# Performance work log

Hardware: AMD Instinct MI355X
Metric: run time of the kernel (lower is better)

## Reference

```python
import jax, jax.numpy as jnp
import numpy as np

# Uniform-scope sizes: B molecules, A atoms/mol, G fragments/mol, W map width,
# H hidden, L attention layers, S = G+1 (fg prompt row prepended per molecule)
B, A, G, W, H, L = 1024, 64, 31, 8, 512, 2
S = G + 1
DK = 32  # attention head dim (hard-coded in the module)


def _layernorm(x, g, b, eps):
    mu = jnp.mean(x, axis=-1, keepdims=True)
    var = jnp.var(x, axis=-1, keepdims=True)
    return g * (x - mu) * jax.lax.rsqrt(var + eps) + b


def setup_inputs() -> dict:
    key = jax.random.key(0)
    ks = jax.random.split(key, 16)
    s = 0.02
    return {
        "f_atom": jax.random.normal(ks[0], (B * A, H), jnp.float32),
        "f_group": jax.random.normal(ks[1], (B * G, H), jnp.float32),
        "fg": jax.random.normal(ks[2], (1, 3 * H), jnp.float32),
        "alpha": 0.1 * jnp.ones((1,), jnp.float32),
        "lr_w": jax.random.normal(ks[3], (3 * H, H), jnp.float32) * s,
        "lr_b": jnp.zeros((H,), jnp.float32),
        "wq_w": jax.random.normal(ks[4], (L, H, DK), jnp.float32) * s,
        "wq_b": jnp.zeros((L, DK), jnp.float32),
        "wk_w": jax.random.normal(ks[5], (L, H, DK), jnp.float32) * s,
        "wk_b": jnp.zeros((L, DK), jnp.float32),
        "wv_w": jax.random.normal(ks[6], (L, H, DK), jnp.float32) * s,
        "wv_b": jnp.zeros((L, DK), jnp.float32),
        "dense_w": jax.random.normal(ks[7], (L, DK, H), jnp.float32) * s,
        "dense_b": jnp.zeros((L, H), jnp.float32),
        "ln_g": jnp.ones((L, H), jnp.float32),
        "ln_b": jnp.zeros((L, H), jnp.float32),
        "lin_w": jax.random.normal(ks[8], (H, H), jnp.float32) * s,
        "lin_b": jnp.zeros((H,), jnp.float32),
        "norm_g": jnp.ones((H,), jnp.float32),
        "norm_b": jnp.zeros((H,), jnp.float32),
        "mapping": jax.random.randint(ks[9], (B * G, W), 0, A + 1, jnp.int64),
    }


def reference(f_atom, f_group, fg, alpha, lr_w, lr_b, wq_w, wq_b, wk_w, wk_b,
              wv_w, wv_b, dense_w, dense_b, ln_g, ln_b, lin_w, lin_b,
              norm_g, norm_b, mapping):
    # --- ragged gather + reduce + pad (vectorized: uniform scopes) ---
    a = f_atom.reshape(B, A, H)
    # prepend zero padding row per molecule (mapping index 0 -> zeros)
    a_pad = jnp.concatenate([jnp.zeros((B, 1, H), a.dtype), a], axis=1)  # [B,A+1,H]
    m = mapping.reshape(B, G, W)
    gathered = a_pad[jnp.arange(B)[:, None, None], m]  # [B,G,W,H]
    g = f_group.reshape(B, G, H)
    cur_g = jnp.concatenate(
        [gathered.sum(axis=2), gathered.max(axis=2), g], axis=-1)  # [B,G,3H]
    brics = jnp.concatenate(
        [jnp.broadcast_to(fg[None], (B, 1, 3 * H)), cur_g], axis=1)  # [B,S,3H]

    f_frag = jax.nn.relu(brics @ lr_w + lr_b)  # [B,S,H]

    # mask built from init_hiddens = f_frag (same for every layer)
    pm = (f_frag != 0).astype(f_frag.dtype)
    mask = jnp.einsum('bsh,bth->bst', pm, pm)  # [B,S,S]
    neg = jnp.asarray(-1e9, f_frag.dtype)
    scale = 1.0 / np.sqrt(DK)

    hs = f_frag
    attn = None
    for l in range(L):
        q = hs @ wq_w[l] + wq_b[l]
        k = hs @ wk_w[l] + wk_b[l]
        v = hs @ wv_w[l] + wv_b[l]
        scores = jnp.einsum('bsd,btd->bst', q, k) * scale
        scores = jnp.where(mask == 0, neg, scores)
        attn = jax.nn.softmax(scores, axis=-1)
        x = jnp.einsum('bst,btd->bsd', attn, v)
        dh = x @ dense_w[l] + dense_b[l]  # dropout is identity in eval
        hs = _layernorm(dh + hs, ln_g[l], ln_b[l], 1e-6)

    f_out = _layernorm(hs @ lin_w + lin_b, norm_g, norm_b, 1e-5) * alpha[0]
    return f_out[:, 0, :], attn
```

## Files before the change

kernel.cpp:

```cpp
#include <hip/hip_runtime.h>

#define B_   1024
#define A_   64
#define G_   31
#define W_   8
#define H_   512
#define L_   2
#define S_   32
#define DK_  32
#define K3H_ 1536

typedef short short8 __attribute__((ext_vector_type(8)));
typedef float floatx4 __attribute__((ext_vector_type(4)));

__device__ __forceinline__ float bf2f(unsigned short u){
  union { unsigned int i; float f; } x; x.i = ((unsigned int)u) << 16; return x.f;
}
__device__ __forceinline__ unsigned short f2bf(float f){
  union { float f; unsigned int i; } x; x.f = f;
  unsigned int u = x.i;
  return (unsigned short)((u + 0x7FFFu + ((u >> 16) & 1u)) >> 16);
}
__device__ __forceinline__ unsigned int pack2bf(float a, float b){
  return (unsigned int)f2bf(a) | ((unsigned int)f2bf(b) << 16);
}
__device__ __forceinline__ void gl_lds16(const unsigned short* g, unsigned short* l){
  __builtin_amdgcn_global_load_lds((const __attribute__((address_space(1))) unsigned int*)g,
                                   (__attribute__((address_space(3))) unsigned int*)l, 16, 0, 0);
}

__global__ __launch_bounds__(256) void prep_weights(
    const float* __restrict__ lr_w, const float* __restrict__ lin_w,
    const float* __restrict__ wq_w, const float* __restrict__ wk_w, const float* __restrict__ wv_w,
    const float* __restrict__ dense_w,
    unsigned short* __restrict__ lr_wT, unsigned short* __restrict__ lin_wT,
    unsigned short* __restrict__ qkvT, unsigned short* __restrict__ denseT){
  int bx = blockIdx.x;
  int tid = threadIdx.x;
  if (bx < 256){
    __shared__ float tile[64][65];
    const float* src; unsigned short* dst; int R, C;
    if (bx < 192){ src = lr_w;  dst = lr_wT;  R = 1536; C = 512; }
    else         { bx -= 192; src = lin_w; dst = lin_wT; R = 512;  C = 512; }
    int rt = bx >> 3, ct = bx & 7;
    int r16 = tid >> 4, c4 = tid & 15;
    #pragma unroll
    for (int p = 0; p < 4; ++p){
      int row = p*16 + r16;
      float4 v = *(const float4*)(src + (size_t)(rt*64 + row) * C + ct*64 + c4*4);
      tile[row][c4*4+0] = v.x; tile[row][c4*4+1] = v.y;
      tile[row][c4*4+2] = v.z; tile[row][c4*4+3] = v.w;
    }
    __syncthreads();
    int rr = tid >> 3, cc8 = tid & 7;
    #pragma unroll
    for (int p = 0; p < 2; ++p){
      int n = p*32 + rr;
      unsigned short o[8] __attribute__((aligned(16)));
      #pragma unroll
      for (int j = 0; j < 8; ++j) o[j] = f2bf(tile[cc8*8 + j][n]);
      *(uint4*)(dst + (size_t)(ct*64 + n) * R + rt*64 + cc8*8) = *(const uint4*)o;
    }
    return;
  }
  int i = (bx - 256) * 256 + tid;
  if (i < 98304){
    int k = i & 511; int t = i >> 9; int n = t & 31; int u = t >> 5;
    int p = u % 3, l = u / 3;
    const float* src = (p == 0) ? wq_w : (p == 1) ? wk_w : wv_w;
    qkvT[((size_t)((l*3+p)*S_ + n)) * H_ + k] = f2bf(src[((size_t)(l*H_ + k)) * DK_ + n]);
    return;
  }
  i -= 98304;
  if (i < 32768){
    int k = i & 31; int t = i >> 5; int n = t & 511; int l = t >> 9;
    denseT[((size_t)(l*H_ + n)) * DK_ + k] = f2bf(dense_w[((size_t)(l*DK_ + k)) * H_ + n]);
  }
}

__global__ __launch_bounds__(256) void build_brics(
    const float* __restrict__ f_atom, const float* __restrict__ f_group,
    const float* __restrict__ fg, const int* __restrict__ mapping,
    unsigned short* __restrict__ brics){
  __shared__ float atoms[64*128];
  int bx = blockIdx.x;
  int b = bx >> 2, qc = bx & 3;
  int kb = qc * 128;
  int tid = threadIdx.x;
  int wave = tid >> 6, lane = tid & 63;
  const float* fa = f_atom + (size_t)b * A_ * H_ + kb;

  #pragma unroll
  for (int j = 0; j < 8; ++j){
    int f = j*256 + tid;
    int r = f >> 5, c4v = f & 31;
    *(float4*)&atoms[r*128 + c4v*4] = *(const float4*)(fa + (size_t)r*H_ + c4v*4);
  }
  __syncthreads();

  int c2 = lane * 2;
  #pragma unroll
  for (int q = 0; q < 8; ++q){
    int s = wave*8 + q;
    unsigned short* out = brics + (size_t)(b*32 + s) * K3H_ + kb;
    if (s == 0){
      #pragma unroll
      for (int t3 = 0; t3 < 3; ++t3){
        const float* fgp = fg + t3*512 + kb + c2;
        *(unsigned int*)(out + t3*512 + c2) = pack2bf(fgp[0], fgp[1]);
      }
    } else {
      int g = s - 1;
      const int* mp = mapping + ((size_t)(b * G_ + g)) * W_;
      int4 m0 = *(const int4*)mp;
      int4 m1 = *(const int4*)(mp + 4);
      int id[8] = {m0.x, m0.y, m0.z, m0.w, m1.x, m1.y, m1.z, m1.w};
      float sum0 = 0.f, sum1 = 0.f;
      float mx0 = -3.4e38f, mx1 = -3.4e38f;
      #pragma unroll
      for (int w = 0; w < 8; ++w){
        int r = id[w] > 0 ? id[w] - 1 : 0;
        float2 v = *(const float2*)&atoms[r*128 + c2];
        bool z = (id[w] == 0);
        float v0 = z ? 0.f : v.x, v1 = z ? 0.f : v.y;
        sum0 += v0; sum1 += v1;
        mx0 = fmaxf(mx0, v0); mx1 = fmaxf(mx1, v1);
      }
      const float* gp = f_group + ((size_t)(b * G_ + g)) * H_ + kb + c2;
      float2 gv = *(const float2*)gp;
      *(unsigned int*)(out + c2)        = pack2bf(sum0, sum1);
      *(unsigned int*)(out + 512 + c2)  = pack2bf(mx0, mx1);
      *(unsigned int*)(out + 1024 + c2) = pack2bf(gv.x, gv.y);
    }
  }
}

__global__ __launch_bounds__(256) void gemm_frag(
    const unsigned short* __restrict__ brics, const unsigned short* __restrict__ wT,
    const float* __restrict__ lr_b, unsigned short* __restrict__ f_frag){
  __shared__ __align__(16) unsigned short As[128*64];
  __shared__ __align__(16) unsigned short Bs[128*64];
  int tid = threadIdx.x;
  int bx = blockIdx.x;
  int xcd = bx & 7, slot = bx >> 3;
  int mtile = xcd + 8 * (slot >> 2);
  int ntile = slot & 3;
  int rowStart = mtile * 128, colStart = ntile * 128;
  int lane = tid & 63, wave = tid >> 6;
  int m16 = lane & 15, quad = lane >> 4;
  int wm = wave >> 1, wn = wave & 1;
  floatx4 acc[4][4];
  #pragma unroll
  for (int i = 0; i < 4; ++i)
    #pragma unroll
    for (int j = 0; j < 4; ++j) acc[i][j] = (floatx4){0.f,0.f,0.f,0.f};

  int srow = tid >> 3;
  int gchunk = (tid & 7) ^ (srow & 7);
  size_t aOff[4], bOff[4];
  #pragma unroll
  for (int p = 0; p < 4; ++p){
    aOff[p] = (size_t)(rowStart + p*32 + srow) * K3H_ + gchunk*8;
    bOff[p] = (size_t)(colStart + p*32 + srow) * K3H_ + gchunk*8;
  }
  int fsw0 = ((0*4 + quad) ^ (m16 & 7)) * 8;
  int fsw1 = ((1*4 + quad) ^ (m16 & 7)) * 8;

  for (int kt = 0; kt < K3H_/64; ++kt){
    int kbase = kt * 64;
    #pragma unroll
    for (int p = 0; p < 4; ++p){
      gl_lds16(brics + aOff[p] + kbase, As + p*2048 + (size_t)tid*8);
      gl_lds16(wT    + bOff[p] + kbase, Bs + p*2048 + (size_t)tid*8);
    }
    __syncthreads();
    #pragma unroll
    for (int ks = 0; ks < 2; ++ks){
      int fsw = ks ? fsw1 : fsw0;
      short8 af[4], bfr[4];
      #pragma unroll
      for (int i = 0; i < 4; ++i){
        af[i]  = *(const short8*)(As + (wm*64 + i*16 + m16)*64 + fsw);
        bfr[i] = *(const short8*)(Bs + (wn*64 + i*16 + m16)*64 + fsw);
      }
      #pragma unroll
      for (int i = 0; i < 4; ++i)
        #pragma unroll
        for (int j = 0; j < 4; ++j)
          acc[i][j] = __builtin_amdgcn_mfma_f32_16x16x32_bf16(af[i], bfr[j], acc[i][j], 0, 0, 0);
    }
    __syncthreads();
  }
  #pragma unroll
  for (int i = 0; i < 4; ++i)
    #pragma unroll
    for (int j = 0; j < 4; ++j){
      int col = colStart + wn*64 + j*16 + m16;
      float bias = lr_b[col];
      #pragma unroll
      for (int r = 0; r < 4; ++r){
        int row = rowStart + wm*64 + i*16 + quad*4 + r;
        float v = acc[i][j][r] + bias;
        v = v > 0.f ? v : 0.f;
        f_frag[(size_t)row * H_ + col] = f2bf(v);
      }
    }
}

__global__ __launch_bounds__(256) void attn_kernel(
    const unsigned short* __restrict__ f_frag,
    const unsigned short* __restrict__ qkvT, const unsigned short* __restrict__ denseT,
    const float* __restrict__ wq_b, const float* __restrict__ wk_b, const float* __restrict__ wv_b,
    const float* __restrict__ dense_b, const float* __restrict__ ln_g, const float* __restrict__ ln_b,
    unsigned short* __restrict__ hsf, float* __restrict__ out_attn){
  const int HP = 544, TP = 40;
  __shared__ __align__(16) unsigned short hs[S_*544];
  __shared__ __align__(16) unsigned short Qs[S_*40];
  __shared__ __align__(16) unsigned short Ks[S_*40];
  __shared__ __align__(16) unsigned short Vt[S_*40];
  __shared__ __align__(16) unsigned short Ps[S_*40];
  __shared__ __align__(16) unsigned short Xs[S_*40];
  __shared__ unsigned long long pmask[S_*8];
  __shared__ unsigned int mz[S_];
  int b = blockIdx.x;
  int tid = threadIdx.x;
  int wave = tid >> 6, lane = tid & 63;
  int m16 = lane & 15, quad = lane >> 4;

  {
    int row = tid >> 3, cc = (tid & 7) * 64;
    const unsigned short* src = f_frag + ((size_t)(b * S_ + row)) * H_ + cc;
    unsigned short* dst = hs + row * HP + cc;
    #pragma unroll
    for (int k = 0; k < 64; k += 8)
      *(uint4*)(dst + k) = *(const uint4*)(src + k);
  }
  if (tid < S_) mz[tid] = 0u;
  __syncthreads();
  {
    int s = tid >> 3, w = tid & 7;
    unsigned long long m = 0ull;
    const unsigned short* hrow = hs + s * HP + w * 64;
    for (int j = 0; j < 64; ++j)
      if (hrow[j] != 0) m |= (1ull << j);
    pmask[s * 8 + w] = m;
  }
  __syncthreads();
  for (int idx = tid; idx < S_*S_; idx += 256){
    int s = idx >> 5, t2 = idx & 31;
    bool inter = false;
    #pragma unroll
    for (int w = 0; w < 8; ++w)
      inter = inter || ((pmask[s*8+w] & pmask[t2*8+w]) != 0ull);
    if (!inter) atomicOr(&mz[s], 1u << t2);
  }
  __syncthreads();

  const float scale = 0.17677669529663687f;
  for (int l = 0; l < L_; ++l){
    {
      int mt = wave >> 1, nt = wave & 1;
      floatx4 aq = {0,0,0,0}, ak = {0,0,0,0}, av = {0,0,0,0};
      const unsigned short* arow = hs + (mt*16 + m16) * HP + quad*8;
      const unsigned short* bq = qkvT + ((size_t)((l*3 + 0)*S_ + nt*16 + m16)) * H_ + quad*8;
      const unsigned short* bk = bq + (size_t)S_ * H_;
      const unsigned short* bv = bk + (size_t)S_ * H_;
      for (int k0 = 0; k0 < H_; k0 += 32){
        short8 a = *(const short8*)(arow + k0);
        aq = __builtin_amdgcn_mfma_f32_16x16x32_bf16(a, *(const short8*)(bq + k0), aq, 0,0,0);
        ak = __builtin_amdgcn_mfma_f32_16x16x32_bf16(a, *(const short8*)(bk + k0), ak, 0,0,0);
        av = __builtin_amdgcn_mfma_f32_16x16x32_bf16(a, *(const short8*)(bv + k0), av, 0,0,0);
      }
      int col = nt*16 + m16;
      float bqs = wq_b[l*DK_ + col], bks = wk_b[l*DK_ + col], bvs = wv_b[l*DK_ + col];
      #pragma unroll
      for (int r = 0; r < 4; ++r){
        int rw = mt*16 + quad*4 + r;
        Qs[rw*TP + col] = f2bf((aq[r] + bqs) * scale);
        Ks[rw*TP + col] = f2bf(ak[r] + bks);
        Vt[col*TP + rw] = f2bf(av[r] + bvs);
      }
    }
    __syncthreads();
    if (wave < 2){
      int mt = wave;
      short8 a  = *(const short8*)(Qs + (mt*16 + m16)*TP + quad*8);
      short8 b0 = *(const short8*)(Ks + m16*TP + quad*8);
      short8 b1 = *(const short8*)(Ks + (16 + m16)*TP + quad*8);
      floatx4 z = {0,0,0,0};
      floatx4 s0 = __builtin_amdgcn_mfma_f32_16x16x32_bf16(a, b0, z, 0,0,0);
      floatx4 s1 = __builtin_amdgcn_mfma_f32_16x16x32_bf16(a, b1, z, 0,0,0);
      #pragma unroll
      for (int r = 0; r < 4; ++r){
        int s = mt*16 + quad*4 + r;
        unsigned int m = mz[s];
        float v0 = ((m >> m16) & 1u) ? -1e9f : s0[r];
        float v1 = ((m >> (16 + m16)) & 1u) ? -1e9f : s1[r];
        float mx = fmaxf(v0, v1);
        #pragma unroll
        for (int d = 1; d < 16; d <<= 1) mx = fmaxf(mx, __shfl_xor(mx, d));
        float e0 = __expf(v0 - mx), e1 = __expf(v1 - mx);
        float sm = e0 + e1;
        #pragma unroll
        for (int d = 1; d < 16; d <<= 1) sm += __shfl_xor(sm, d);
        float inv = 1.f / sm;
        float p0 = e0 * inv, p1 = e1 * inv;
        Ps[s*TP + m16] = f2bf(p0);
        Ps[s*TP + 16 + m16] = f2bf(p1);
        if (l == L_ - 1){
          float* oa = out_attn + ((size_t)b * S_ + s) * S_;
          oa[m16] = p0; oa[16 + m16] = p1;
        }
      }
    }
    __syncthreads();
    {
      int mt = wave >> 1, nt = wave & 1;
      short8 a  = *(const short8*)(Ps + (mt*16 + m16)*TP + quad*8);
      short8 bv = *(const short8*)(Vt + (nt*16 + m16)*TP + quad*8);
      floatx4 z = {0,0,0,0};
      floatx4 x = __builtin_amdgcn_mfma_f32_16x16x32_bf16(a, bv, z, 0,0,0);
      #pragma unroll
      for (int r = 0; r < 4; ++r)
        Xs[(mt*16 + quad*4 + r)*TP + nt*16 + m16] = f2bf(x[r]);
    }
    __syncthreads();
    {
      short8 ax0 = *(const short8*)(Xs + m16*TP + quad*8);
      short8 ax1 = *(const short8*)(Xs + (16 + m16)*TP + quad*8);
      #pragma unroll
      for (int j = 0; j < 8; ++j){
        int col = (wave*8 + j)*16 + m16;
        short8 bw = *(const short8*)(denseT + ((size_t)(l*H_ + col)) * DK_ + quad*8);
        float db = dense_b[l*H_ + col];
        floatx4 z = {0,0,0,0};
        floatx4 d0 = __builtin_amdgcn_mfma_f32_16x16x32_bf16(ax0, bw, z, 0,0,0);
        floatx4 d1 = __builtin_amdgcn_mfma_f32_16x16x32_bf16(ax1, bw, z, 0,0,0);
        #pragma unroll
        for (int r = 0; r < 4; ++r){
          int row0 = quad*4 + r;
          float y0 = d0[r] + db + bf2f(hs[row0*HP + col]);
          hs[row0*HP + col] = f2bf(y0);
          int row1 = 16 + quad*4 + r;
          float y1 = d1[r] + db + bf2f(hs[row1*HP + col]);
          hs[row1*HP + col] = f2bf(y1);
        }
      }
    }
    __syncthreads();
    {
      #pragma unroll
      for (int rr = 0; rr < 8; ++rr){
        int row = wave*8 + rr;
        unsigned short* hrow = hs + row*HP + lane*8;
        short8 hv = *(const short8*)hrow;
        float v[8]; float s1 = 0.f, s2 = 0.f;
        #pragma unroll
        for (int j = 0; j < 8; ++j){ v[j] = bf2f((unsigned short)hv[j]); s1 += v[j]; s2 += v[j]*v[j]; }
        #pragma unroll
        for (int d = 1; d < 64; d <<= 1){ s1 += __shfl_xor(s1, d); s2 += __shfl_xor(s2, d); }
        float mean = s1 * (1.f/512.f);
        float var = s2 * (1.f/512.f) - mean*mean;
        float rs = rsqrtf(var + 1e-6f);
        unsigned short o[8] __attribute__((aligned(16)));
        #pragma unroll
        for (int j = 0; j < 8; ++j){
          int colj = lane*8 + j;
          float nv = (v[j] - mean) * rs * ln_g[l*H_ + colj] + ln_b[l*H_ + colj];
          o[j] = f2bf(nv);
        }
        *(uint4*)hrow = *(const uint4*)o;
      }
    }
    __syncthreads();
  }
  if (tid < 64){
    *(uint4*)(hsf + (size_t)b * H_ + tid*8) = *(const uint4*)(hs + tid*8);
  }
}

__global__ __launch_bounds__(256) void final_kernel(
    const unsigned short* __restrict__ hsf, const unsigned short* __restrict__ lin_wT,
    const float* __restrict__ lin_b, const float* __restrict__ norm_g, const float* __restrict__ norm_b,
    const float* __restrict__ alpha, float* __restrict__ out_f){
  const int HP = 544;
  __shared__ __align__(16) unsigned short hsb[32*544];
  int blk = blockIdx.x;
  int tid = threadIdx.x;
  int wave = tid >> 6, lane = tid & 63;
  int m16 = lane & 15, quad = lane >> 4;
  {
    int row = tid >> 3, cc = (tid & 7) * 64;
    const unsigned short* src = hsf + ((size_t)(blk*32 + row)) * H_ + cc;
    unsigned short* dst = hsb + row*HP + cc;
    #pragma unroll
    for (int k = 0; k < 64; k += 8)
      *(uint4*)(dst + k) = *(const uint4*)(src + k);
  }
  __syncthreads();
  floatx4 acc[2][8];
  #pragma unroll
  for (int mt = 0; mt < 2; ++mt)
    #pragma unroll
    for (int j = 0; j < 8; ++j) acc[mt][j] = (floatx4){0.f,0.f,0.f,0.f};
  for (int k0 = 0; k0 < H_; k0 += 32){
    short8 a0 = *(const short8*)(hsb + m16*HP + k0 + quad*8);
    short8 a1 = *(const short8*)(hsb + (16 + m16)*HP + k0 + quad*8);
    #pragma unroll
    for (int j = 0; j < 8; ++j){
      int n = (wave*8 + j)*16 + m16;
      short8 bw = *(const short8*)(lin_wT + (size_t)n * H_ + k0 + quad*8);
      acc[0][j] = __builtin_amdgcn_mfma_f32_16x16x32_bf16(a0, bw, acc[0][j], 0,0,0);
      acc[1][j] = __builtin_amdgcn_mfma_f32_16x16x32_bf16(a1, bw, acc[1][j], 0,0,0);
    }
  }
  __syncthreads();
  #pragma unroll
  for (int mt = 0; mt < 2; ++mt)
    #pragma unroll
    for (int j = 0; j < 8; ++j){
      int col = (wave*8 + j)*16 + m16;
      float lb = lin_b[col];
      #pragma unroll
      for (int r = 0; r < 4; ++r){
        int row = mt*16 + quad*4 + r;
        hsb[row*HP + col] = f2bf(acc[mt][j][r] + lb);
      }
    }
  __syncthreads();
  float al = alpha[0];
  #pragma unroll
  for (int rr = 0; rr < 8; ++rr){
    int row = wave*8 + rr;
    const unsigned short* hrow = hsb + row*HP + lane*8;
    short8 hv = *(const short8*)hrow;
    float v[8]; float s1 = 0.f, s2 = 0.f;
    #pragma unroll
    for (int j = 0; j < 8; ++j){ v[j] = bf2f((unsigned short)hv[j]); s1 += v[j]; s2 += v[j]*v[j]; }
    #pragma unroll
    for (int d = 1; d < 64; d <<= 1){ s1 += __shfl_xor(s1, d); s2 += __shfl_xor(s2, d); }
    float mean = s1 * (1.f/512.f);
    float var = s2 * (1.f/512.f) - mean*mean;
    float rs = rsqrtf(var + 1e-5f);
    float o[8];
    #pragma unroll
    for (int j = 0; j < 8; ++j){
      int colj = lane*8 + j;
      o[j] = ((v[j] - mean) * rs * norm_g[colj] + norm_b[colj]) * al;
    }
    float* op = out_f + ((size_t)(blk*32 + row)) * H_ + lane*8;
    float4 f0 = {o[0], o[1], o[2], o[3]};
    float4 f1 = {o[4], o[5], o[6], o[7]};
    *(float4*)op = f0;
    *(float4*)(op + 4) = f1;
  }
}

extern "C" void kernel_launch(void* const* d_in, const int* in_sizes, int n_in,
                              void* d_out, int out_size, void* d_ws, size_t ws_size,
                              hipStream_t stream){
  const float* f_atom  = (const float*)d_in[0];
  const float* f_group = (const float*)d_in[1];
  const float* fg      = (const float*)d_in[2];
  const float* alpha   = (const float*)d_in[3];
  const float* lr_w    = (const float*)d_in[4];
  const float* lr_b    = (const float*)d_in[5];
  const float* wq_w    = (const float*)d_in[6];
  const float* wq_b    = (const float*)d_in[7];
  const float* wk_w    = (const float*)d_in[8];
  const float* wk_b    = (const float*)d_in[9];
  const float* wv_w    = (const float*)d_in[10];
  const float* wv_b    = (const float*)d_in[11];
  const float* dense_w = (const float*)d_in[12];
  const float* dense_b = (const float*)d_in[13];
  const float* ln_g    = (const float*)d_in[14];
  const float* ln_b    = (const float*)d_in[15];
  const float* lin_w   = (const float*)d_in[16];
  const float* lin_b   = (const float*)d_in[17];
  const float* norm_g  = (const float*)d_in[18];
  const float* norm_b  = (const float*)d_in[19];
  const int*   mapping = (const int*)d_in[20];

  unsigned short* brics  = (unsigned short*)d_ws;
  unsigned short* f_frag = brics  + (size_t)32768 * 1536;
  unsigned short* lr_wT  = f_frag + (size_t)32768 * 512;
  unsigned short* qkvT   = lr_wT  + (size_t)512 * 1536;
  unsigned short* denseT = qkvT   + (size_t)2*3*32*512;
  unsigned short* lin_wT = denseT + (size_t)2*512*32;
  unsigned short* hsf    = lin_wT + (size_t)512*512;

  float* out_f    = (float*)d_out;
  float* out_attn = out_f + (size_t)B_ * H_;

  prep_weights<<<768, 256, 0, stream>>>(lr_w, lin_w, wq_w, wk_w, wv_w, dense_w,
                                        lr_wT, lin_wT, qkvT, denseT);
  build_brics<<<B_ * 4, 256, 0, stream>>>(f_atom, f_group, fg, mapping, brics);
  gemm_frag<<<(32768/128) * (512/128), 256, 0, stream>>>(brics, lr_wT, lr_b, f_frag);
  attn_kernel<<<B_, 256, 0, stream>>>(f_frag, qkvT, denseT, wq_b, wk_b, wv_b,
                                      dense_b, ln_g, ln_b, hsf, out_attn);
  final_kernel<<<B_/32, 256, 0, stream>>>(hsf, lin_wT, lin_b, norm_g, norm_b, alpha, out_f);
}
```

Measured before the change: 475.6 us.

## Merge weight prep with brics build and vectorize attention epilogue accesses

Folds the weight transposition/conversion kernel and the brics gather/reduce kernel into one launch with a shared LDS buffer, removing a kernel launch and letting the two independent workloads run concurrently. In the attention kernel, the nonzero-mask scan now uses 16-byte vector loads instead of scalar loads. The dense projection MFMA swaps its operands so each lane holds four consecutive columns, which allows 8-byte residual reads/writes and a float4 bias load instead of scattered scalar LDS accesses. The merged kernel's LDS footprint is set by the larger 32 KB brics buffer, which may limit occupancy for the transpose blocks.

```diff
diff --git a/kernel.cpp b/kernel.cpp
--- a/kernel.cpp
+++ b/kernel.cpp
@@ -29,27 +29,82 @@
                                    (__attribute__((address_space(3))) unsigned int*)l, 16, 0, 0);
 }
 
-__global__ __launch_bounds__(256) void prep_weights(
+__global__ __launch_bounds__(256) void prep_and_build(
+    const float* __restrict__ f_atom, const float* __restrict__ f_group,
+    const float* __restrict__ fg, const int* __restrict__ mapping,
     const float* __restrict__ lr_w, const float* __restrict__ lin_w,
     const float* __restrict__ wq_w, const float* __restrict__ wk_w, const float* __restrict__ wv_w,
     const float* __restrict__ dense_w,
+    unsigned short* __restrict__ brics,
     unsigned short* __restrict__ lr_wT, unsigned short* __restrict__ lin_wT,
     unsigned short* __restrict__ qkvT, unsigned short* __restrict__ denseT){
+  __shared__ __align__(16) float ldsf[8192];
   int bx = blockIdx.x;
   int tid = threadIdx.x;
-  if (bx < 256){
-    __shared__ float tile[64][65];
+
+  if (bx < 4096){
+    int b = bx >> 2, qc = bx & 3;
+    int kb = qc * 128;
+    int wave = tid >> 6, lane = tid & 63;
+    const float* fa = f_atom + (size_t)b * A_ * H_ + kb;
+    #pragma unroll
+    for (int j = 0; j < 8; ++j){
+      int f = j*256 + tid;
+      int r = f >> 5, c4v = f & 31;
+      *(float4*)&ldsf[r*128 + c4v*4] = *(const float4*)(fa + (size_t)r*H_ + c4v*4);
+    }
+    __syncthreads();
+    int c2 = lane * 2;
+    #pragma unroll
+    for (int q = 0; q < 8; ++q){
+      int s = wave*8 + q;
+      unsigned short* out = brics + (size_t)(b*32 + s) * K3H_ + kb;
+      if (s == 0){
+        #pragma unroll
+        for (int t3 = 0; t3 < 3; ++t3){
+          const float* fgp = fg + t3*512 + kb + c2;
+          *(unsigned int*)(out + t3*512 + c2) = pack2bf(fgp[0], fgp[1]);
+        }
+      } else {
+        int g = s - 1;
+        const int* mp = mapping + ((size_t)(b * G_ + g)) * W_;
+        int4 m0 = *(const int4*)mp;
+        int4 m1 = *(const int4*)(mp + 4);
+        int id[8] = {m0.x, m0.y, m0.z, m0.w, m1.x, m1.y, m1.z, m1.w};
+        float sum0 = 0.f, sum1 = 0.f;
+        float mx0 = -3.4e38f, mx1 = -3.4e38f;
+        #pragma unroll
+        for (int w = 0; w < 8; ++w){
+          int r = id[w] > 0 ? id[w] - 1 : 0;
+          float2 v = *(const float2*)&ldsf[r*128 + c2];
+          bool z = (id[w] == 0);
+          float v0 = z ? 0.f : v.x, v1 = z ? 0.f : v.y;
+          sum0 += v0; sum1 += v1;
+          mx0 = fmaxf(mx0, v0); mx1 = fmaxf(mx1, v1);
+        }
+        const float* gp = f_group + ((size_t)(b * G_ + g)) * H_ + kb + c2;
+        float2 gv = *(const float2*)gp;
+        *(unsigned int*)(out + c2)        = pack2bf(sum0, sum1);
+        *(unsigned int*)(out + 512 + c2)  = pack2bf(mx0, mx1);
+        *(unsigned int*)(out + 1024 + c2) = pack2bf(gv.x, gv.y);
+      }
+    }
+    return;
+  }
+
+  if (bx < 4352){
+    int tb = bx - 4096;
     const float* src; unsigned short* dst; int R, C;
-    if (bx < 192){ src = lr_w;  dst = lr_wT;  R = 1536; C = 512; }
-    else         { bx -= 192; src = lin_w; dst = lin_wT; R = 512;  C = 512; }
-    int rt = bx >> 3, ct = bx & 7;
+    if (tb < 192){ src = lr_w;  dst = lr_wT;  R = 1536; C = 512; }
+    else         { tb -= 192; src = lin_w; dst = lin_wT; R = 512;  C = 512; }
+    int rt = tb >> 3, ct = tb & 7;
     int r16 = tid >> 4, c4 = tid & 15;
     #pragma unroll
     for (int p = 0; p < 4; ++p){
       int row = p*16 + r16;
       float4 v = *(const float4*)(src + (size_t)(rt*64 + row) * C + ct*64 + c4*4);
-      tile[row][c4*4+0] = v.x; tile[row][c4*4+1] = v.y;
-      tile[row][c4*4+2] = v.z; tile[row][c4*4+3] = v.w;
+      ldsf[row*65 + c4*4+0] = v.x; ldsf[row*65 + c4*4+1] = v.y;
+      ldsf[row*65 + c4*4+2] = v.z; ldsf[row*65 + c4*4+3] = v.w;
     }
     __syncthreads();
     int rr = tid >> 3, cc8 = tid & 7;
@@ -58,12 +113,13 @@
       int n = p*32 + rr;
       unsigned short o[8] __attribute__((aligned(16)));
       #pragma unroll
-      for (int j = 0; j < 8; ++j) o[j] = f2bf(tile[cc8*8 + j][n]);
+      for (int j = 0; j < 8; ++j) o[j] = f2bf(ldsf[(cc8*8 + j)*65 + n]);
       *(uint4*)(dst + (size_t)(ct*64 + n) * R + rt*64 + cc8*8) = *(const uint4*)o;
     }
     return;
   }
-  int i = (bx - 256) * 256 + tid;
+
+  int i = (bx - 4352) * 256 + tid;
   if (i < 98304){
     int k = i & 511; int t = i >> 9; int n = t & 31; int u = t >> 5;
     int p = u % 3, l = u / 3;
@@ -75,63 +131,6 @@
   if (i < 32768){
     int k = i & 31; int t = i >> 5; int n = t & 511; int l = t >> 9;
     denseT[((size_t)(l*H_ + n)) * DK_ + k] = f2bf(dense_w[((size_t)(l*DK_ + k)) * H_ + n]);
-  }
-}
-
-__global__ __launch_bounds__(256) void build_brics(
-    const float* __restrict__ f_atom, const float* __restrict__ f_group,
-    const float* __restrict__ fg, const int* __restrict__ mapping,
-    unsigned short* __restrict__ brics){
-  __shared__ float atoms[64*128];
-  int bx = blockIdx.x;
-  int b = bx >> 2, qc = bx & 3;
-  int kb = qc * 128;
-  int tid = threadIdx.x;
-  int wave = tid >> 6, lane = tid & 63;
-  const float* fa = f_atom + (size_t)b * A_ * H_ + kb;
-
-  #pragma unroll
-  for (int j = 0; j < 8; ++j){
-    int f = j*256 + tid;
-    int r = f >> 5, c4v = f & 31;
-    *(float4*)&atoms[r*128 + c4v*4] = *(const float4*)(fa + (size_t)r*H_ + c4v*4);
-  }
-  __syncthreads();
-
-  int c2 = lane * 2;
-  #pragma unroll
-  for (int q = 0; q < 8; ++q){
-    int s = wave*8 + q;
-    unsigned short* out = brics + (size_t)(b*32 + s) * K3H_ + kb;
-    if (s == 0){
-      #pragma unroll
-      for (int t3 = 0; t3 < 3; ++t3){
-        const float* fgp = fg + t3*512 + kb + c2;
-        *(unsigned int*)(out + t3*512 + c2) = pack2bf(fgp[0], fgp[1]);
-      }
-    } else {
-      int g = s - 1;
-      const int* mp = mapping + ((size_t)(b * G_ + g)) * W_;
-      int4 m0 = *(const int4*)mp;
-      int4 m1 = *(const int4*)(mp + 4);
-      int id[8] = {m0.x, m0.y, m0.z, m0.w, m1.x, m1.y, m1.z, m1.w};
-      float sum0 = 0.f, sum1 = 0.f;
-      float mx0 = -3.4e38f, mx1 = -3.4e38f;
-      #pragma unroll
-      for (int w = 0; w < 8; ++w){
-        int r = id[w] > 0 ? id[w] - 1 : 0;
-        float2 v = *(const float2*)&atoms[r*128 + c2];
-        bool z = (id[w] == 0);
-        float v0 = z ? 0.f : v.x, v1 = z ? 0.f : v.y;
-        sum0 += v0; sum1 += v1;
-        mx0 = fmaxf(mx0, v0); mx1 = fmaxf(mx1, v1);
-      }
-      const float* gp = f_group + ((size_t)(b * G_ + g)) * H_ + kb + c2;
-      float2 gv = *(const float2*)gp;
-      *(unsigned int*)(out + c2)        = pack2bf(sum0, sum1);
-      *(unsigned int*)(out + 512 + c2)  = pack2bf(mx0, mx1);
-      *(unsigned int*)(out + 1024 + c2) = pack2bf(gv.x, gv.y);
-    }
   }
 }
 
@@ -239,10 +238,15 @@
   __syncthreads();
   {
     int s = tid >> 3, w = tid & 7;
+    const unsigned short* hrow = hs + s * HP + w * 64;
     unsigned long long m = 0ull;
-    const unsigned short* hrow = hs + s * HP + w * 64;
-    for (int j = 0; j < 64; ++j)
-      if (hrow[j] != 0) m |= (1ull << j);
+    #pragma unroll
+    for (int c = 0; c < 64; c += 8){
+      short8 hv = *(const short8*)(hrow + c);
+      #pragma unroll
+      for (int j = 0; j < 8; ++j)
+        if ((unsigned short)hv[j] != 0) m |= (1ull << (c + j));
+    }
     pmask[s * 8 + w] = m;
   }
   __syncthreads();
@@ -326,25 +330,32 @@
     }
     __syncthreads();
     {
-      short8 ax0 = *(const short8*)(Xs + m16*TP + quad*8);
-      short8 ax1 = *(const short8*)(Xs + (16 + m16)*TP + quad*8);
+      short8 bx0 = *(const short8*)(Xs + m16*TP + quad*8);
+      short8 bx1 = *(const short8*)(Xs + (16 + m16)*TP + quad*8);
       #pragma unroll
       for (int j = 0; j < 8; ++j){
-        int col = (wave*8 + j)*16 + m16;
-        short8 bw = *(const short8*)(denseT + ((size_t)(l*H_ + col)) * DK_ + quad*8);
-        float db = dense_b[l*H_ + col];
+        int dct = wave*8 + j;
+        short8 aw = *(const short8*)(denseT + ((size_t)(l*H_ + dct*16 + m16)) * DK_ + quad*8);
         floatx4 z = {0,0,0,0};
-        floatx4 d0 = __builtin_amdgcn_mfma_f32_16x16x32_bf16(ax0, bw, z, 0,0,0);
-        floatx4 d1 = __builtin_amdgcn_mfma_f32_16x16x32_bf16(ax1, bw, z, 0,0,0);
+        floatx4 d0 = __builtin_amdgcn_mfma_f32_16x16x32_bf16(aw, bx0, z, 0,0,0);
+        floatx4 d1 = __builtin_amdgcn_mfma_f32_16x16x32_bf16(aw, bx1, z, 0,0,0);
+        int dc0 = dct*16 + quad*4;
+        float4 db4 = *(const float4*)(dense_b + l*H_ + dc0);
+        const float dbr[4] = {db4.x, db4.y, db4.z, db4.w};
+        unsigned short* h0 = hs + m16*HP + dc0;
+        unsigned short* h1 = hs + (16 + m16)*HP + dc0;
+        unsigned long long u0 = *(unsigned long long*)h0;
+        unsigned long long u1 = *(unsigned long long*)h1;
+        unsigned long long o0 = 0ull, o1 = 0ull;
         #pragma unroll
         for (int r = 0; r < 4; ++r){
-          int row0 = quad*4 + r;
-          float y0 = d0[r] + db + bf2f(hs[row0*HP + col]);
-          hs[row0*HP + col] = f2bf(y0);
-          int row1 = 16 + quad*4 + r;
-          float y1 = d1[r] + db + bf2f(hs[row1*HP + col]);
-          hs[row1*HP + col] = f2bf(y1);
+          float hv0 = bf2f((unsigned short)(u0 >> (16*r)));
+          float hv1 = bf2f((unsigned short)(u1 >> (16*r)));
+          o0 |= (unsigned long long)f2bf(d0[r] + dbr[r] + hv0) << (16*r);
+          o1 |= (unsigned long long)f2bf(d1[r] + dbr[r] + hv1) << (16*r);
         }
+        *(unsigned long long*)h0 = o0;
+        *(unsigned long long*)h1 = o1;
       }
     }
     __syncthreads();
@@ -492,9 +503,9 @@
   float* out_f    = (float*)d_out;
   float* out_attn = out_f + (size_t)B_ * H_;
 
-  prep_weights<<<768, 256, 0, stream>>>(lr_w, lin_w, wq_w, wk_w, wv_w, dense_w,
-                                        lr_wT, lin_wT, qkvT, denseT);
-  build_brics<<<B_ * 4, 256, 0, stream>>>(f_atom, f_group, fg, mapping, brics);
+  prep_and_build<<<4864, 256, 0, stream>>>(f_atom, f_group, fg, mapping,
+                                           lr_w, lin_w, wq_w, wk_w, wv_w, dense_w,
+                                           brics, lr_wT, lin_wT, qkvT, denseT);
   gemm_frag<<<(32768/128) * (512/128), 256, 0, stream>>>(brics, lr_wT, lr_b, f_frag);
   attn_kernel<<<B_, 256, 0, stream>>>(f_frag, qkvT, denseT, wq_b, wk_b, wv_b,
                                       dense_b, ln_g, ln_b, hsf, out_attn);
```

Result: faster. 464.7 us (-2.3%).
